# Performance work log

Measured on AMD Instinct MI355X. Metric: run time of the kernel, lower is better.

Reference implementation:

```python
import jax, jax.numpy as jnp
import numpy as np

B, T, C = 2, 2048, 2048
H = 16
ROPE_DIM, NOPE_DIM, V_DIM = 64, 64, 128
HEAD_DIM = NOPE_DIM + ROPE_DIM  # 128
Q_RANK, KV_RANK = 1536, 512


def setup_inputs() -> dict:
    key = jax.random.key(0)
    ks = jax.random.split(key, 8)
    std = 0.02
    return {
        "x": jax.random.normal(ks[0], (B, T, C), jnp.float32),
        "cos": jax.random.normal(ks[1], (1, T, 1, ROPE_DIM // 2), jnp.float32),
        "sin": jax.random.normal(ks[2], (1, T, 1, ROPE_DIM // 2), jnp.float32),
        "wq_down": jax.random.normal(ks[3], (Q_RANK, C), jnp.float32) * std,
        "wq_up": jax.random.normal(ks[4], (H * HEAD_DIM, Q_RANK), jnp.float32) * std,
        "wkv_down": jax.random.normal(ks[5], (KV_RANK, C), jnp.float32) * std,
        "wkv_up": jax.random.normal(ks[6], (H * (HEAD_DIM + V_DIM), KV_RANK), jnp.float32) * std,
        "wo": jax.random.normal(ks[7], (C, H * V_DIM), jnp.float32) * std,
    }


def _rope(x, cos, sin):
    # x: [B, T, H, rope_dim]
    d = x.shape[-1] // 2
    x1, x2 = x[..., :d], x[..., d:]
    return jnp.concatenate([x1 * cos + x2 * sin, -x1 * sin + x2 * cos], axis=-1)


def _rms_norm(x):
    eps = jnp.finfo(x.dtype).eps
    return x * jax.lax.rsqrt(jnp.mean(jnp.square(x), axis=-1, keepdims=True) + eps)


def reference(x, cos, sin, wq_down, wq_up, wkv_down, wkv_up, wo):
    # Low-rank q projection
    q = jnp.einsum('btc,rc,dr->btd', x, wq_down, wq_up)
    q = q.reshape(B, T, H, HEAD_DIM)
    q_nope, q_rope = q[..., :NOPE_DIM], q[..., NOPE_DIM:]
    # Low-rank kv projection (naive decompression)
    kv = jnp.einsum('btc,rc,dr->btd', x, wkv_down, wkv_up)
    kv = kv.reshape(B, T, H, HEAD_DIM + V_DIM)
    k_nope = kv[..., :NOPE_DIM]
    k_rope = kv[..., NOPE_DIM:HEAD_DIM]
    v = kv[..., HEAD_DIM:]
    # Partial RoPE on the rope sub-dims only
    q_rope = _rope(q_rope, cos, sin)
    k_rope = _rope(k_rope, cos, sin)
    q = _rms_norm(jnp.concatenate([q_nope, q_rope], axis=-1))
    k = _rms_norm(jnp.concatenate([k_nope, k_rope], axis=-1))
    # Causal SDPA: [B, H, T, T]
    scale = 1.0 / jnp.sqrt(jnp.float32(HEAD_DIM))
    scores = jnp.einsum('bthd,bshd->bhts', q, k) * scale
    causal = jnp.tril(jnp.ones((T, T), dtype=bool))
    scores = jnp.where(causal, scores, jnp.finfo(scores.dtype).min)
    probs = jax.nn.softmax(scores, axis=-1)
    y = jnp.einsum('bhts,bshd->bthd', probs, v).reshape(B, T, H * V_DIM)
    return y @ wo.T
```

## Files before the change

kernel.cpp:

```cpp
#include <hip/hip_runtime.h>
#include <hip/hip_bf16.h>
#include <math.h>
#include <type_traits>

#define AS1 __attribute__((address_space(1)))
#define AS3 __attribute__((address_space(3)))

typedef __bf16  bf16x8 __attribute__((ext_vector_type(8)));
typedef float   f32x4  __attribute__((ext_vector_type(4)));
typedef __hip_bfloat16 bf16;

#define MFMA16x16x32 __builtin_amdgcn_mfma_f32_16x16x32_bf16

__device__ __forceinline__ void gload16(const void* g, void* l) {
  __builtin_amdgcn_global_load_lds((const AS1 void*)g, (AS3 void*)l, 16, 0, 0);
}

__device__ __forceinline__ unsigned short bfbits(float v) {
  return __builtin_bit_cast(unsigned short, __float2bfloat16(v));
}

#define LGKM0 __asm__ volatile("s_waitcnt lgkmcnt(0)" ::: "memory")
#define BARRIER __builtin_amdgcn_s_barrier()

struct CastArgs {
  const float4* src[6];
  ushort4* dst[6];
  unsigned bound[6];
};

__global__ __launch_bounds__(256) void f2bf_multi(CastArgs a) {
  unsigned i = blockIdx.x * 256 + threadIdx.x;
  if (i >= a.bound[5]) return;
  unsigned lo = 0;
  int s = 0;
#pragma unroll
  for (int k = 0; k < 5; k++) {
    if (i >= a.bound[k]) { s = k + 1; lo = a.bound[k]; }
  }
  unsigned idx = i - lo;
  float4 v = a.src[s][idx];
  ushort4 o;
  o.x = bfbits(v.x); o.y = bfbits(v.y); o.z = bfbits(v.z); o.w = bfbits(v.w);
  a.dst[s][idx] = o;
}

template <int BM, int BN, typename OutT, bool KVUP>
__global__ __launch_bounds__(512, 2) void gemm256(const bf16* __restrict__ A,
                                                  const bf16* __restrict__ W,
                                                  OutT* __restrict__ Cp,
                                                  bf16* __restrict__ vT,
                                                  int N, int K, int lda) {
  constexpr int WGN = (BN == 256) ? 4 : 2;
  constexpr int WGM = 8 / WGN;
  constexpr int MF = BM / WGM / 16;
  constexpr int NF = BN / WGN / 16;
  constexpr int LA = BM / 128;
  constexpr int LB = BN / 128;
  constexpr int L  = LA + LB;
  constexpr int ASUB = BM * 64;
  constexpr int BSUB = BN * 64;
  __shared__ __align__(16) char lds[4 * (ASUB + BSUB)];
  char* ldsA = lds;
  char* ldsB = lds + 4 * ASUB;

  const int t = threadIdx.x, w = t >> 6, lane = t & 63;
  const int quad = lane >> 4, l16 = lane & 15;
  const int wm = w / WGN, wn = w % WGN;
  const int wrow = wm * (BM / WGM), wcol = wn * (BN / WGN);
  const size_t m0 = (size_t)blockIdx.x * BM;
  const size_t n0 = (size_t)blockIdx.y * BN;
  const int NT = K / 32;

  const bf16* asrc[LA];
#pragma unroll
  for (int st = 0; st < LA; ++st) {
    int slot = st * 512 + w * 64 + lane;
    int row = slot % BM, chunk = slot / BM;
    asrc[st] = A + (m0 + row) * (size_t)lda + chunk * 8;
  }
  const bf16* bsrc[LB];
#pragma unroll
  for (int st = 0; st < LB; ++st) {
    int slot = st * 512 + w * 64 + lane;
    int row = slot % BN, chunk = slot / BN;
    bsrc[st] = W + (n0 + row) * (size_t)K + chunk * 8;
  }

  auto stage = [&](int s, int c) {
#pragma unroll
    for (int st = 0; st < LA; ++st)
      gload16(asrc[st] + s * 32, ldsA + c * ASUB + st * 8192 + w * 1024);
#pragma unroll
    for (int st = 0; st < LB; ++st)
      gload16(bsrc[st] + s * 32, ldsB + c * BSUB + st * 8192 + w * 1024);
  };

  f32x4 acc[MF][NF];
#pragma unroll
  for (int i = 0; i < MF; i++)
#pragma unroll
    for (int j = 0; j < NF; j++) acc[i][j] = f32x4{0.f, 0.f, 0.f, 0.f};

  auto compute = [&](int c) {
    bf16x8 af[MF], bw[NF];
#pragma unroll
    for (int nf = 0; nf < NF; ++nf)
      bw[nf] = *(const bf16x8*)(ldsB + c * BSUB +
                                (quad * BN + wcol + nf * 16 + l16) * 16);
#pragma unroll
    for (int mf = 0; mf < MF; ++mf)
      af[mf] = *(const bf16x8*)(ldsA + c * ASUB +
                                (quad * BM + wrow + mf * 16 + l16) * 16);
    __builtin_amdgcn_s_setprio(1);
#pragma unroll
    for (int mf = 0; mf < MF; ++mf)
#pragma unroll
      for (int nf = 0; nf < NF; ++nf)
        acc[mf][nf] = MFMA16x16x32(af[mf], bw[nf], acc[mf][nf], 0, 0, 0);
    __builtin_amdgcn_s_setprio(0);
  };

#define VM_STEADY do { if constexpr (L == 4) \
    __asm__ volatile("s_waitcnt vmcnt(12)" ::: "memory"); \
  else __asm__ volatile("s_waitcnt vmcnt(9)" ::: "memory"); } while (0)
#define VM_2 do { if constexpr (L == 4) \
    __asm__ volatile("s_waitcnt vmcnt(8)" ::: "memory"); \
  else __asm__ volatile("s_waitcnt vmcnt(6)" ::: "memory"); } while (0)
#define VM_1 do { if constexpr (L == 4) \
    __asm__ volatile("s_waitcnt vmcnt(4)" ::: "memory"); \
  else __asm__ volatile("s_waitcnt vmcnt(3)" ::: "memory"); } while (0)
#define VM_0 __asm__ volatile("s_waitcnt vmcnt(0)" ::: "memory")

  stage(0, 0); stage(1, 1); stage(2, 2);

  for (int s4 = 0; s4 < NT - 4; s4 += 4) {
#pragma unroll
    for (int jj = 0; jj < 4; ++jj) {
      stage(s4 + jj + 3, (jj + 3) & 3);
      VM_STEADY;
      BARRIER;
      compute(jj);
      LGKM0;
      BARRIER;
    }
  }
  stage(NT - 1, 3);
  VM_STEADY; BARRIER; compute(0); LGKM0; BARRIER;
  VM_2;      BARRIER; compute(1); LGKM0; BARRIER;
  VM_1;      BARRIER; compute(2); LGKM0; BARRIER;
  VM_0;      BARRIER; compute(3);

#undef VM_STEADY
#undef VM_2
#undef VM_1
#undef VM_0

  if constexpr (!KVUP) {
#pragma unroll
    for (int mf = 0; mf < MF; ++mf)
#pragma unroll
      for (int nf = 0; nf < NF; ++nf)
#pragma unroll
        for (int r = 0; r < 4; ++r) {
          size_t row = m0 + wrow + mf * 16 + quad * 4 + r;
          size_t col = n0 + wcol + nf * 16 + l16;
          float v = acc[mf][nf][r];
          if constexpr (std::is_same<OutT, float>::value)
            Cp[row * N + col] = v;
          else
            Cp[row * N + col] = __float2bfloat16(v);
        }
  } else {
    const int head = (int)(n0 >> 8);
    if (wcol < 128) {
#pragma unroll
      for (int mf = 0; mf < MF; ++mf)
#pragma unroll
        for (int nf = 0; nf < NF; ++nf)
#pragma unroll
          for (int r = 0; r < 4; ++r) {
            size_t row = m0 + wrow + mf * 16 + quad * 4 + r;
            size_t col = n0 + wcol + nf * 16 + l16;
            Cp[row * 4096 + col] = __float2bfloat16(acc[mf][nf][r]);
          }
    } else {
#pragma unroll
      for (int mf = 0; mf < MF; ++mf) {
        size_t row = m0 + wrow + mf * 16 + quad * 4;
        int bb = (int)(row >> 11), tloc = (int)(row & 2047);
#pragma unroll
        for (int nf = 0; nf < NF; ++nf) {
          int d = wcol - 128 + nf * 16 + l16;
          ushort4 v4;
          v4.x = bfbits(acc[mf][nf][0]);
          v4.y = bfbits(acc[mf][nf][1]);
          v4.z = bfbits(acc[mf][nf][2]);
          v4.w = bfbits(acc[mf][nf][3]);
          *(ushort4*)(vT + ((size_t)(bb * 16 + head) * 128 + d) * 2048 + tloc) = v4;
        }
      }
    }
  }
}

__global__ __launch_bounds__(256) void rope_rms(const bf16* __restrict__ qraw,
                                                const bf16* __restrict__ kvraw,
                                                const float* __restrict__ cosp,
                                                const float* __restrict__ sinp,
                                                bf16* __restrict__ qn,
                                                bf16* __restrict__ kn) {
  const int bt = blockIdx.x;
  const int w = threadIdx.x >> 6, lane = threadIdx.x & 63;
  const int h = blockIdx.y * 4 + w;
  const int tt = bt & 2047;
  const float c = cosp[tt * 32 + (lane & 31)];
  const float s = sinp[tt * 32 + (lane & 31)];
  const float inv128 = 1.0f / 128.0f;
  const float eps = 1.1920929e-7f;

  {
    const bf16* base = qraw + (size_t)bt * 2048 + h * 128;
    float a = (float)base[lane];
    float o = (float)base[64 + lane];
    float partner = __shfl_xor(o, 32);
    float orope = (lane < 32) ? (o * c + partner * s) : (o * c - partner * s);
    float ss = a * a + orope * orope;
#pragma unroll
    for (int off = 1; off < 64; off <<= 1) ss += __shfl_xor(ss, off);
    float rn = rsqrtf(ss * inv128 + eps);
    bf16* outp = qn + ((size_t)bt * 16 + h) * 128;
    outp[lane] = __float2bfloat16(a * rn);
    outp[64 + lane] = __float2bfloat16(orope * rn);
  }
  {
    const bf16* base = kvraw + (size_t)bt * 4096 + h * 256;
    float a = (float)base[lane];
    float o = (float)base[64 + lane];
    float partner = __shfl_xor(o, 32);
    float orope = (lane < 32) ? (o * c + partner * s) : (o * c - partner * s);
    float ss = a * a + orope * orope;
#pragma unroll
    for (int off = 1; off < 64; off <<= 1) ss += __shfl_xor(ss, off);
    float rn = rsqrtf(ss * inv128 + eps);
    bf16* outp = kn + ((size_t)bt * 16 + h) * 128;
    outp[lane] = __float2bfloat16(a * rn);
    outp[64 + lane] = __float2bfloat16(orope * rn);
  }
}

__global__ __launch_bounds__(256, 2) void attn_kernel(const bf16* __restrict__ qn,
                                                      const bf16* __restrict__ kn,
                                                      const bf16* __restrict__ vT,
                                                      bf16* __restrict__ y) {
  __shared__ __align__(16) bf16 Ks[2 * 64 * 128];
  __shared__ __align__(16) bf16 Vs[2 * 128 * 64];
  __shared__ __align__(16) bf16 Ps[4 * 16 * 64];
  const int t = threadIdx.x, w = t >> 6, lane = t & 63;
  const int quad = lane >> 4, l16 = lane & 15;
  const int b = blockIdx.x >> 4, h = blockIdx.x & 15;
  const int pr = (int)blockIdx.y;
  const int T_ = 2048, H_ = 16;
  const float K1 = 0.08838834764831845f * 1.4426950408889634f;
  const float K2 = -12.0f * 1.4426950408889634f;

  const int cgk = l16 ^ ((w * 4 + quad) & 7);
  const char* kg0 = (const char*)(kn + ((size_t)(b * T_) * H_ + h) * 128)
                    + (size_t)(w * 4 + quad) * 4096 + (size_t)cgk * 16;
  const int vrow = w * 8 + (lane >> 3);
  const int cgv = (lane & 7) ^ (vrow & 7);
  const char* vg0 = (const char*)(vT + ((size_t)(b * H_ + h) * 128 + vrow) * T_)
                    + (size_t)cgv * 16;

  auto stage = [&](auto bufc, int it2) {
    constexpr int BUF = decltype(bufc)::value;
    const size_t koff = (size_t)it2 * 262144;
    const size_t voff = (size_t)it2 * 128;
#pragma unroll
    for (int is = 0; is < 4; ++is)
      gload16(kg0 + koff + (size_t)is * 65536,
              (char*)Ks + BUF * 16384 + is * 4096 + w * 1024);
#pragma unroll
    for (int is = 0; is < 4; ++is)
      gload16(vg0 + voff + (size_t)is * 131072,
              (char*)Vs + BUF * 16384 + is * 4096 + w * 1024);
  };

  auto body = [&](auto bufc, int it, int nt, int xb,
                  bf16x8* qf, f32x4* yacc, float* lrow) {
    constexpr int BUF = decltype(bufc)::value;
    if (it + 1 < nt) {
      stage(std::integral_constant<int, 1 - BUF>{}, it + 1);
      __asm__ volatile("s_waitcnt vmcnt(8)" ::: "memory");
    } else {
      __asm__ volatile("s_waitcnt vmcnt(0)" ::: "memory");
    }
    __asm__ volatile("s_barrier" ::: "memory");

    f32x4 sacc[4];
#pragma unroll
    for (int cg = 0; cg < 4; cg++) sacc[cg] = f32x4{0.f, 0.f, 0.f, 0.f};
    __builtin_amdgcn_s_setprio(1);
#pragma unroll
    for (int cg = 0; cg < 4; ++cg) {
#pragma unroll
      for (int ks = 0; ks < 4; ++ks) {
        const int pos = (ks * 4 + quad) ^ (l16 & 7);
        const bf16x8 kf = *(const bf16x8*)((const char*)Ks + BUF * 16384 +
                                           (cg * 16 + l16) * 256 + pos * 16);
        sacc[cg] = MFMA16x16x32(qf[ks], kf, sacc[cg], 0, 0, 0);
      }
    }
    __builtin_amdgcn_s_setprio(0);

    const bool diag = (it == xb);
    float p[4][4];
#pragma unroll
    for (int cg = 0; cg < 4; ++cg)
#pragma unroll
      for (int r = 0; r < 4; ++r) {
        float e;
        if (diag && (cg * 16 + l16 > w * 16 + quad * 4 + r))
          e = 0.0f;
        else
          e = exp2f(fmaf(sacc[cg][r], K1, K2));
        p[cg][r] = e;
        lrow[r] += e;
      }

#pragma unroll
    for (int cg = 0; cg < 4; cg++)
#pragma unroll
      for (int r = 0; r < 4; r++) {
        const int row = quad * 4 + r;
        const int col = cg * 16 + l16;
        Ps[w * 1024 + row * 64 + (((col >> 3) ^ (row & 7)) << 3) + (col & 7)] =
            __float2bfloat16(p[cg][r]);
      }
    __asm__ volatile("s_waitcnt lgkmcnt(0)" ::: "memory");

    bf16x8 pf[2];
#pragma unroll
    for (int k2 = 0; k2 < 2; k2++)
      pf[k2] = *(const bf16x8*)(&Ps[w * 1024 + l16 * 64 +
                                    (((k2 * 4 + quad) ^ (l16 & 7)) << 3)]);
    __builtin_amdgcn_s_setprio(1);
#pragma unroll
    for (int dg = 0; dg < 8; dg++) {
#pragma unroll
      for (int k2 = 0; k2 < 2; k2++) {
        const int pos = (k2 * 4 + quad) ^ (l16 & 7);
        const bf16x8 vf = *(const bf16x8*)((const char*)Vs + BUF * 16384 +
                                           (dg * 16 + l16) * 128 + pos * 16);
        yacc[dg] = MFMA16x16x32(pf[k2], vf, yacc[dg], 0, 0, 0);
      }
    }
    __builtin_amdgcn_s_setprio(0);
    __asm__ volatile("s_barrier" ::: "memory");
  };

  const std::integral_constant<int, 0> c0{};
  const std::integral_constant<int, 1> c1{};

  for (int sidx = 0; sidx < 2; ++sidx) {
    const int xb = sidx ? pr : (31 - pr);
    const int q0 = xb * 64;
    const int nt = xb + 1;

    bf16x8 qf[4];
    {
      const bf16* qbase = qn + ((size_t)(b * T_ + q0 + w * 16 + l16) * H_ + h) * 128;
#pragma unroll
      for (int ks = 0; ks < 4; ks++) qf[ks] = *(const bf16x8*)(qbase + ks * 32 + quad * 8);
    }
    f32x4 yacc[8];
#pragma unroll
    for (int i = 0; i < 8; i++) yacc[i] = f32x4{0.f, 0.f, 0.f, 0.f};
    float lrow[4] = {0.f, 0.f, 0.f, 0.f};

    stage(c0, 0);
    int it = 0;
    for (; it + 2 <= nt; it += 2) {
      body(c0, it, nt, xb, qf, yacc, lrow);
      body(c1, it + 1, nt, xb, qf, yacc, lrow);
    }
    if (it < nt) body(c0, it, nt, xb, qf, yacc, lrow);

#pragma unroll
    for (int off = 1; off < 16; off <<= 1)
#pragma unroll
      for (int r = 0; r < 4; r++) lrow[r] += __shfl_xor(lrow[r], off);
#pragma unroll
    for (int r = 0; r < 4; r++) {
      float inv = 1.0f / lrow[r];
      size_t qrow = (size_t)(b * T_ + q0 + w * 16 + quad * 4 + r);
      bf16* outp = y + qrow * 2048 + h * 128;
#pragma unroll
      for (int dg = 0; dg < 8; dg++)
        outp[dg * 16 + l16] = __float2bfloat16(yacc[dg][r] * inv);
    }
  }
}

extern "C" void kernel_launch(void* const* d_in, const int* in_sizes, int n_in,
                              void* d_out, int out_size, void* d_ws, size_t ws_size,
                              hipStream_t stream) {
  (void)in_sizes; (void)n_in; (void)out_size; (void)ws_size;
  const float* x    = (const float*)d_in[0];
  const float* cosp = (const float*)d_in[1];
  const float* sinp = (const float*)d_in[2];
  const float* wqd  = (const float*)d_in[3];
  const float* wqu  = (const float*)d_in[4];
  const float* wkvd = (const float*)d_in[5];
  const float* wkvu = (const float*)d_in[6];
  const float* wo   = (const float*)d_in[7];
  float* out = (float*)d_out;

  char* ws = (char*)d_ws;
  size_t off = 0;
  auto alloc = [&](size_t elems) { bf16* p = (bf16*)(ws + off); off += elems * 2; return p; };
  bf16* xb      = alloc((size_t)4096 * 2048);
  bf16* wqdB    = alloc((size_t)1536 * 2048);
  bf16* wkvdB   = alloc((size_t)512 * 2048);
  bf16* wquB    = alloc((size_t)2048 * 1536);
  bf16* wkvuB   = alloc((size_t)4096 * 512);
  bf16* woB     = alloc((size_t)2048 * 2048);
  bf16* qkvdown = alloc((size_t)4096 * 2048);
  bf16* qraw    = alloc((size_t)4096 * 2048);
  bf16* kvraw   = alloc((size_t)4096 * 4096);
  bf16* qnb     = alloc((size_t)4096 * 16 * 128);
  bf16* knb     = alloc((size_t)4096 * 16 * 128);
  bf16* vTb     = alloc((size_t)2 * 16 * 128 * 2048);
  bf16* yb      = alloc((size_t)4096 * 2048);

  CastArgs ca;
  const float* srcs[6] = {x, wqd, wkvd, wqu, wkvu, wo};
  bf16* dsts[6]        = {xb, wqdB, wkvdB, wquB, wkvuB, woB};
  size_t cnts[6] = {(size_t)4096 * 2048, (size_t)1536 * 2048, (size_t)512 * 2048,
                    (size_t)2048 * 1536, (size_t)4096 * 512,  (size_t)2048 * 2048};
  unsigned cum = 0;
  for (int i = 0; i < 6; i++) {
    ca.src[i] = (const float4*)srcs[i];
    ca.dst[i] = (ushort4*)dsts[i];
    cum += (unsigned)(cnts[i] / 4);
    ca.bound[i] = cum;
  }
  f2bf_multi<<<dim3((cum + 255) / 256), 256, 0, stream>>>(ca);

  gemm256<256, 128, bf16, false><<<dim3(16, 16), 512, 0, stream>>>(
      xb, wqdB, qkvdown, nullptr, 2048, 2048, 2048);
  gemm256<256, 128, bf16, false><<<dim3(16, 16), 512, 0, stream>>>(
      qkvdown, wquB, qraw, nullptr, 2048, 1536, 2048);
  gemm256<256, 256, bf16, true><<<dim3(16, 16), 512, 0, stream>>>(
      qkvdown + 1536, wkvuB, kvraw, vTb, 4096, 512, 2048);
  rope_rms<<<dim3(4096, 4), 256, 0, stream>>>(qraw, kvraw, cosp, sinp, qnb, knb);
  attn_kernel<<<dim3(32, 16), 256, 0, stream>>>(qnb, knb, vTb, yb);
  gemm256<256, 128, float, false><<<dim3(16, 16), 512, 0, stream>>>(
      yb, woB, out, nullptr, 2048, 2048, 2048);
}
```

Before: 451.2 us.

## Replace GEMM with 256x256 eight-phase pipelined kernel using swizzled LDS

Replaces the templated 4-stage GEMM with a fixed 256x256 tile kernel that uses a K-tile of 64, double-buffers LDS at 128KB, and XOR-swizzles the LDS chunk layout to avoid bank conflicts. Each iteration interleaves half-tile global->LDS loads with eight MFMA clusters and register prefetch, so loads overlap compute. The GEMMs that used 256x128 tiles now use 256x256 tiles, which halves their grid to 128 blocks. That may underfill the GPU's CUs and raises register pressure.

New measurement: 400.2 us. 1.13x faster.

```diff
diff --git a/kernel.cpp b/kernel.cpp
--- a/kernel.cpp
+++ b/kernel.cpp
@@ -22,6 +22,7 @@
 
 #define LGKM0 __asm__ volatile("s_waitcnt lgkmcnt(0)" ::: "memory")
 #define BARRIER __builtin_amdgcn_s_barrier()
+#define VMCNT(n) __asm__ volatile("s_waitcnt vmcnt(" #n ")" ::: "memory")
 
 struct CastArgs {
   const float4* src[6];
@@ -45,126 +46,169 @@
   a.dst[s][idx] = o;
 }
 
-template <int BM, int BN, typename OutT, bool KVUP>
-__global__ __launch_bounds__(512, 2) void gemm256(const bf16* __restrict__ A,
-                                                  const bf16* __restrict__ W,
-                                                  OutT* __restrict__ Cp,
-                                                  bf16* __restrict__ vT,
-                                                  int N, int K, int lda) {
-  constexpr int WGN = (BN == 256) ? 4 : 2;
-  constexpr int WGM = 8 / WGN;
-  constexpr int MF = BM / WGM / 16;
-  constexpr int NF = BN / WGN / 16;
-  constexpr int LA = BM / 128;
-  constexpr int LB = BN / 128;
-  constexpr int L  = LA + LB;
-  constexpr int ASUB = BM * 64;
-  constexpr int BSUB = BN * 64;
-  __shared__ __align__(16) char lds[4 * (ASUB + BSUB)];
-  char* ldsA = lds;
-  char* ldsB = lds + 4 * ASUB;
-
+template <typename OutT, bool KVUP>
+__global__ __launch_bounds__(512, 2) void gemm8p(const bf16* __restrict__ A,
+                                                 const bf16* __restrict__ W,
+                                                 OutT* __restrict__ Cp,
+                                                 bf16* __restrict__ vT,
+                                                 int N, int K, int lda) {
+  __shared__ __align__(16) char lds[131072];
   const int t = threadIdx.x, w = t >> 6, lane = t & 63;
   const int quad = lane >> 4, l16 = lane & 15;
-  const int wm = w / WGN, wn = w % WGN;
-  const int wrow = wm * (BM / WGM), wcol = wn * (BN / WGN);
-  const size_t m0 = (size_t)blockIdx.x * BM;
-  const size_t n0 = (size_t)blockIdx.y * BN;
-  const int NT = K / 32;
-
-  const bf16* asrc[LA];
-#pragma unroll
-  for (int st = 0; st < LA; ++st) {
-    int slot = st * 512 + w * 64 + lane;
-    int row = slot % BM, chunk = slot / BM;
-    asrc[st] = A + (m0 + row) * (size_t)lda + chunk * 8;
-  }
-  const bf16* bsrc[LB];
-#pragma unroll
-  for (int st = 0; st < LB; ++st) {
-    int slot = st * 512 + w * 64 + lane;
-    int row = slot % BN, chunk = slot / BN;
-    bsrc[st] = W + (n0 + row) * (size_t)K + chunk * 8;
-  }
-
-  auto stage = [&](int s, int c) {
-#pragma unroll
-    for (int st = 0; st < LA; ++st)
-      gload16(asrc[st] + s * 32, ldsA + c * ASUB + st * 8192 + w * 1024);
-#pragma unroll
-    for (int st = 0; st < LB; ++st)
-      gload16(bsrc[st] + s * 32, ldsB + c * BSUB + st * 8192 + w * 1024);
-  };
-
-  f32x4 acc[MF][NF];
-#pragma unroll
-  for (int i = 0; i < MF; i++)
-#pragma unroll
-    for (int j = 0; j < NF; j++) acc[i][j] = f32x4{0.f, 0.f, 0.f, 0.f};
-
-  auto compute = [&](int c) {
-    bf16x8 af[MF], bw[NF];
-#pragma unroll
-    for (int nf = 0; nf < NF; ++nf)
-      bw[nf] = *(const bf16x8*)(ldsB + c * BSUB +
-                                (quad * BN + wcol + nf * 16 + l16) * 16);
-#pragma unroll
-    for (int mf = 0; mf < MF; ++mf)
-      af[mf] = *(const bf16x8*)(ldsA + c * ASUB +
-                                (quad * BM + wrow + mf * 16 + l16) * 16);
+  const int wr = w >> 2, wc = w & 3;
+  const size_t m0 = (size_t)blockIdx.x * 256;
+  const size_t n0 = (size_t)blockIdx.y * 256;
+  const int NI = K >> 7;
+
+  const int srow = w * 8 + (lane >> 3);
+  const int schunk = (lane & 7) ^ ((lane >> 3) & 7);
+  const bf16* aS = A + (m0 + srow) * (size_t)lda + schunk * 8;
+  const bf16* bS = W + (n0 + srow) * (size_t)K + schunk * 8;
+
+  auto stageA = [&](int kt, int h) {
+    const bf16* src = aS + (size_t)(h * 128) * lda + kt * 64;
+    char* dst = lds + (kt & 1) * 32768 + h * 16384 + w * 1024;
+    gload16(src, dst);
+    gload16(src + (size_t)64 * lda, dst + 8192);
+  };
+  auto stageB = [&](int kt, int h) {
+    const bf16* src = bS + (size_t)(h * 128) * K + kt * 64;
+    char* dst = lds + 65536 + (kt & 1) * 32768 + h * 16384 + w * 1024;
+    gload16(src, dst);
+    gload16(src + (size_t)64 * K, dst + 8192);
+  };
+
+  const int cq0 = ((quad) ^ (l16 & 7)) * 16;
+  const int cq1 = ((4 + quad) ^ (l16 & 7)) * 16;
+  const char* aRb = lds + wr * 16384 + l16 * 128;
+  const char* bRb = lds + 65536 + (wc >> 1) * 16384 + ((wc & 1) * 64 + l16) * 128;
+  auto rdA = [&](int sl, int mf, int kh) -> bf16x8 {
+    return *(const bf16x8*)(aRb + sl * 32768 + mf * 2048 + (kh ? cq1 : cq0));
+  };
+  auto rdB = [&](int sl, int nf, int kh) -> bf16x8 {
+    return *(const bf16x8*)(bRb + sl * 32768 + nf * 2048 + (kh ? cq1 : cq0));
+  };
+
+  bf16x8 aR[8][2], bR[4][2];
+  f32x4 acc[8][4];
+#pragma unroll
+  for (int i = 0; i < 8; i++)
+#pragma unroll
+    for (int j = 0; j < 4; j++) acc[i][j] = f32x4{0.f, 0.f, 0.f, 0.f};
+
+  auto cluster = [&](int mh, int nh) {
     __builtin_amdgcn_s_setprio(1);
 #pragma unroll
-    for (int mf = 0; mf < MF; ++mf)
-#pragma unroll
-      for (int nf = 0; nf < NF; ++nf)
-        acc[mf][nf] = MFMA16x16x32(af[mf], bw[nf], acc[mf][nf], 0, 0, 0);
+    for (int m2 = 0; m2 < 4; ++m2)
+#pragma unroll
+      for (int n2 = 0; n2 < 2; ++n2)
+#pragma unroll
+        for (int kh = 0; kh < 2; ++kh)
+          acc[mh * 4 + m2][nh * 2 + n2] =
+              MFMA16x16x32(aR[mh * 4 + m2][kh], bR[nh * 2 + n2][kh],
+                           acc[mh * 4 + m2][nh * 2 + n2], 0, 0, 0);
     __builtin_amdgcn_s_setprio(0);
   };
 
-#define VM_STEADY do { if constexpr (L == 4) \
-    __asm__ volatile("s_waitcnt vmcnt(12)" ::: "memory"); \
-  else __asm__ volatile("s_waitcnt vmcnt(9)" ::: "memory"); } while (0)
-#define VM_2 do { if constexpr (L == 4) \
-    __asm__ volatile("s_waitcnt vmcnt(8)" ::: "memory"); \
-  else __asm__ volatile("s_waitcnt vmcnt(6)" ::: "memory"); } while (0)
-#define VM_1 do { if constexpr (L == 4) \
-    __asm__ volatile("s_waitcnt vmcnt(4)" ::: "memory"); \
-  else __asm__ volatile("s_waitcnt vmcnt(3)" ::: "memory"); } while (0)
-#define VM_0 __asm__ volatile("s_waitcnt vmcnt(0)" ::: "memory")
-
-  stage(0, 0); stage(1, 1); stage(2, 2);
-
-  for (int s4 = 0; s4 < NT - 4; s4 += 4) {
-#pragma unroll
-    for (int jj = 0; jj < 4; ++jj) {
-      stage(s4 + jj + 3, (jj + 3) & 3);
-      VM_STEADY;
-      BARRIER;
-      compute(jj);
-      LGKM0;
-      BARRIER;
-    }
-  }
-  stage(NT - 1, 3);
-  VM_STEADY; BARRIER; compute(0); LGKM0; BARRIER;
-  VM_2;      BARRIER; compute(1); LGKM0; BARRIER;
-  VM_1;      BARRIER; compute(2); LGKM0; BARRIER;
-  VM_0;      BARRIER; compute(3);
-
-#undef VM_STEADY
-#undef VM_2
-#undef VM_1
-#undef VM_0
+  stageA(0, 0); stageA(0, 1); stageB(0, 0); stageB(0, 1);
+  stageA(1, 0); stageA(1, 1); stageB(1, 0); stageB(1, 1);
+  VMCNT(8);
+  BARRIER;
+#pragma unroll
+  for (int mf = 0; mf < 4; ++mf)
+#pragma unroll
+    for (int kh = 0; kh < 2; ++kh) aR[mf][kh] = rdA(0, mf, kh);
+#pragma unroll
+  for (int nf = 0; nf < 2; ++nf)
+#pragma unroll
+    for (int kh = 0; kh < 2; ++kh) bR[nf][kh] = rdB(0, nf, kh);
+
+  for (int i = 0; i < NI; ++i) {
+    const int kt1 = 2 * i + 1, kt2 = 2 * i + 2, kt3 = 2 * i + 3;
+    const bool hn = (i + 1 < NI);
+
+#pragma unroll
+    for (int kh = 0; kh < 2; ++kh) { bR[2][kh] = rdB(0, 2, kh); bR[3][kh] = rdB(0, 3, kh); }
+    if (i > 0) stageB(kt1, 0);
+    BARRIER; LGKM0;
+    cluster(0, 0);
+    BARRIER;
+
+#pragma unroll
+    for (int mf = 0; mf < 4; ++mf)
+#pragma unroll
+      for (int kh = 0; kh < 2; ++kh) aR[4 + mf][kh] = rdA(0, 4 + mf, kh);
+    if (i > 0) stageB(kt1, 1);
+    BARRIER; LGKM0;
+    cluster(0, 1);
+    BARRIER;
+
+    if (hn) stageA(kt2, 0);
+    BARRIER; LGKM0;
+    cluster(1, 0);
+    if (hn) { VMCNT(2); } else { VMCNT(0); }
+    BARRIER;
+
+#pragma unroll
+    for (int mf = 0; mf < 4; ++mf)
+#pragma unroll
+      for (int kh = 0; kh < 2; ++kh) aR[mf][kh] = rdA(1, mf, kh);
+#pragma unroll
+    for (int nf = 0; nf < 2; ++nf)
+#pragma unroll
+      for (int kh = 0; kh < 2; ++kh) bR[nf][kh] = rdB(1, nf, kh);
+    if (hn) stageA(kt2, 1);
+    BARRIER; LGKM0;
+    cluster(1, 1);
+    BARRIER;
+
+#pragma unroll
+    for (int kh = 0; kh < 2; ++kh) { bR[2][kh] = rdB(1, 2, kh); bR[3][kh] = rdB(1, 3, kh); }
+    if (hn) stageB(kt2, 0);
+    BARRIER; LGKM0;
+    cluster(0, 0);
+    BARRIER;
+
+#pragma unroll
+    for (int mf = 0; mf < 4; ++mf)
+#pragma unroll
+      for (int kh = 0; kh < 2; ++kh) aR[4 + mf][kh] = rdA(1, 4 + mf, kh);
+    if (hn) stageB(kt2, 1);
+    BARRIER; LGKM0;
+    cluster(0, 1);
+    BARRIER;
+
+    if (hn) stageA(kt3, 0);
+    BARRIER; LGKM0;
+    cluster(1, 0);
+    if (hn) { VMCNT(2); }
+    BARRIER;
+
+    if (hn) {
+#pragma unroll
+      for (int mf = 0; mf < 4; ++mf)
+#pragma unroll
+        for (int kh = 0; kh < 2; ++kh) aR[mf][kh] = rdA(0, mf, kh);
+#pragma unroll
+      for (int nf = 0; nf < 2; ++nf)
+#pragma unroll
+        for (int kh = 0; kh < 2; ++kh) bR[nf][kh] = rdB(0, nf, kh);
+      stageA(kt3, 1);
+    }
+    BARRIER; LGKM0;
+    cluster(1, 1);
+    BARRIER;
+  }
 
   if constexpr (!KVUP) {
 #pragma unroll
-    for (int mf = 0; mf < MF; ++mf)
-#pragma unroll
-      for (int nf = 0; nf < NF; ++nf)
+    for (int mf = 0; mf < 8; ++mf)
+#pragma unroll
+      for (int nf = 0; nf < 4; ++nf)
 #pragma unroll
         for (int r = 0; r < 4; ++r) {
-          size_t row = m0 + wrow + mf * 16 + quad * 4 + r;
-          size_t col = n0 + wcol + nf * 16 + l16;
+          size_t row = m0 + wr * 128 + mf * 16 + quad * 4 + r;
+          size_t col = n0 + wc * 64 + nf * 16 + l16;
           float v = acc[mf][nf][r];
           if constexpr (std::is_same<OutT, float>::value)
             Cp[row * N + col] = v;
@@ -173,25 +217,25 @@
         }
   } else {
     const int head = (int)(n0 >> 8);
-    if (wcol < 128) {
-#pragma unroll
-      for (int mf = 0; mf < MF; ++mf)
-#pragma unroll
-        for (int nf = 0; nf < NF; ++nf)
+    if (wc < 2) {
+#pragma unroll
+      for (int mf = 0; mf < 8; ++mf)
+#pragma unroll
+        for (int nf = 0; nf < 4; ++nf)
 #pragma unroll
           for (int r = 0; r < 4; ++r) {
-            size_t row = m0 + wrow + mf * 16 + quad * 4 + r;
-            size_t col = n0 + wcol + nf * 16 + l16;
+            size_t row = m0 + wr * 128 + mf * 16 + quad * 4 + r;
+            size_t col = n0 + wc * 64 + nf * 16 + l16;
             Cp[row * 4096 + col] = __float2bfloat16(acc[mf][nf][r]);
           }
     } else {
 #pragma unroll
-      for (int mf = 0; mf < MF; ++mf) {
-        size_t row = m0 + wrow + mf * 16 + quad * 4;
+      for (int mf = 0; mf < 8; ++mf) {
+        size_t row = m0 + wr * 128 + mf * 16 + quad * 4;
         int bb = (int)(row >> 11), tloc = (int)(row & 2047);
 #pragma unroll
-        for (int nf = 0; nf < NF; ++nf) {
-          int d = wcol - 128 + nf * 16 + l16;
+        for (int nf = 0; nf < 4; ++nf) {
+          int d = (wc - 2) * 64 + nf * 16 + l16;
           ushort4 v4;
           v4.x = bfbits(acc[mf][nf][0]);
           v4.y = bfbits(acc[mf][nf][1]);
@@ -447,14 +491,14 @@
   }
   f2bf_multi<<<dim3((cum + 255) / 256), 256, 0, stream>>>(ca);
 
-  gemm256<256, 128, bf16, false><<<dim3(16, 16), 512, 0, stream>>>(
+  gemm8p<bf16, false><<<dim3(16, 8), 512, 0, stream>>>(
       xb, wqdB, qkvdown, nullptr, 2048, 2048, 2048);
-  gemm256<256, 128, bf16, false><<<dim3(16, 16), 512, 0, stream>>>(
+  gemm8p<bf16, false><<<dim3(16, 8), 512, 0, stream>>>(
       qkvdown, wquB, qraw, nullptr, 2048, 1536, 2048);
-  gemm256<256, 256, bf16, true><<<dim3(16, 16), 512, 0, stream>>>(
+  gemm8p<bf16, true><<<dim3(16, 16), 512, 0, stream>>>(
       qkvdown + 1536, wkvuB, kvraw, vTb, 4096, 512, 2048);
   rope_rms<<<dim3(4096, 4), 256, 0, stream>>>(qraw, kvraw, cosp, sinp, qnb, knb);
   attn_kernel<<<dim3(32, 16), 256, 0, stream>>>(qnb, knb, vTb, yb);
-  gemm256<256, 128, float, false><<<dim3(16, 16), 512, 0, stream>>>(
+  gemm8p<float, false><<<dim3(16, 8), 512, 0, stream>>>(
       yb, woB, out, nullptr, 2048, 2048, 2048);
 }
```
